# Kernel optimization log

Hardware: AMD Instinct MI355X
Metric: run time of the kernel (lower is better)

Reference implementation:

```python
import jax, jax.numpy as jnp
import numpy as np

D = 256; H = 8; DK = 32; L = 5; FF = 2048; K = 31
EPS_LN = 1e-12  # espnet LayerNorm eps
EPS_BN = 1e-5   # torch BatchNorm1d eps


def _ln(x, g, b):
    mu = x.mean(-1, keepdims=True)
    v = ((x - mu) ** 2).mean(-1, keepdims=True)
    return (x - mu) / jnp.sqrt(v + EPS_LN) * g + b


def _swish(x):
    return x * jax.nn.sigmoid(x)


def _pos_emb(T):
    # espnet RelPositionalEncoding: relative positions T-1 .. -(T-1), length 2T-1
    pos = jnp.arange(T, dtype=jnp.float32)[:, None]
    div = jnp.exp(jnp.arange(0, D, 2, dtype=jnp.float32) * (-np.log(10000.0) / D))[None, :]
    pe_pos = jnp.stack([jnp.sin(pos * div), jnp.cos(pos * div)], -1).reshape(T, D)
    pe_neg = jnp.stack([jnp.sin(-pos * div), jnp.cos(-pos * div)], -1).reshape(T, D)
    return jnp.concatenate([pe_pos[::-1], pe_neg[1:]], 0)  # (2T-1, D)


def _rel_shift(x):
    # x: (B, H, T, 2T-1) -> (B, H, T, T), Transformer-XL style shift
    B, Hh, T, N = x.shape
    x = jnp.pad(x, ((0, 0), (0, 0), (0, 0), (1, 0)))
    x = x.reshape(B, Hh, N + 1, T)[:, :, 1:, :].reshape(B, Hh, T, N)
    return x[..., : (N // 2 + 1)]


def _attn(x, pe, mask, Wq, bq, Wk, bk, Wv, bv, Wo, bo, Wp, pu, pv):
    B, T, _ = x.shape
    q = (x @ Wq.T + bq).reshape(B, T, H, DK)
    k = (x @ Wk.T + bk).reshape(B, T, H, DK).transpose(0, 2, 1, 3)
    v = (x @ Wv.T + bv).reshape(B, T, H, DK).transpose(0, 2, 1, 3)
    p = (pe @ Wp.T).reshape(-1, H, DK)  # (2T-1, H, DK)
    qu = (q + pu).transpose(0, 2, 1, 3)
    qv = (q + pv).transpose(0, 2, 1, 3)
    ac = jnp.einsum('bhtd,bhsd->bhts', qu, k)
    bd = _rel_shift(jnp.einsum('bhtd,nhd->bhtn', qv, p))
    scores = (ac + bd) / np.sqrt(DK)
    m = mask[:, None, :, :]  # (B,1,1,T)
    scores = jnp.where(m, scores, -1e30)
    a = jax.nn.softmax(scores, -1)
    a = jnp.where(m, a, 0.0)
    out = jnp.einsum('bhts,bhsd->bthd', a, v).reshape(B, T, D)
    return out @ Wo.T + bo


def _conv(x, pw1_w, pw1_b, dw_w, dw_b, bn_g, bn_b, pw2_w, pw2_b):
    y = x @ pw1_w.T + pw1_b                      # (B,T,2D)
    a, b = jnp.split(y, 2, -1)
    y = (a * jax.nn.sigmoid(b)).transpose(0, 2, 1)  # GLU -> (B,D,T)
    y = jax.lax.conv_general_dilated(
        y, dw_w[:, None, :], (1,), [(K // 2, K // 2)],
        feature_group_count=D, dimension_numbers=('NCW', 'OIW', 'NCW')
    ) + dw_b[None, :, None]
    mu = y.mean((0, 2), keepdims=True)
    var = ((y - mu) ** 2).mean((0, 2), keepdims=True)  # batch stats (train mode)
    y = (y - mu) / jnp.sqrt(var + EPS_BN) * bn_g[None, :, None] + bn_b[None, :, None]
    y = _swish(y).transpose(0, 2, 1)
    return y @ pw2_w.T + pw2_b


def _forward(xs, Wemb, bemb, ln_in_g, ln_in_b, Wq, bq, Wk, bk, Wv, bv, Wo, bo, Wp,
             pos_u, pos_v, ln1_g, ln1_b, lnc_g, lnc_b, lnf_g, lnf_b, lnfin_g, lnfin_b,
             pw1_w, pw1_b, dw_w, dw_b, bn_g, bn_b, pw2_w, pw2_b,
             ff1_w, ff1_b, ff2_w, ff2_b, after_g, after_b, mask):
    B, T, _ = xs.shape
    x = _ln(xs @ Wemb.T + bemb, ln_in_g, ln_in_b)  # linear input layer + LN
    x = x * np.sqrt(D)                              # rel-pos encoding x-scale
    pe = _pos_emb(T)
    for i in range(L):
        x = x + _attn(_ln(x, ln1_g[i], ln1_b[i]), pe, mask,
                      Wq[i], bq[i], Wk[i], bk[i], Wv[i], bv[i], Wo[i], bo[i],
                      Wp[i], pos_u[i], pos_v[i])
        x = x + _conv(_ln(x, lnc_g[i], lnc_b[i]),
                      pw1_w[i], pw1_b[i], dw_w[i], dw_b[i],
                      bn_g[i], bn_b[i], pw2_w[i], pw2_b[i])
        h = _ln(x, lnf_g[i], lnf_b[i])
        x = x + _swish(h @ ff1_w[i].T + ff1_b[i]) @ ff2_w[i].T + ff2_b[i]
        x = _ln(x, lnfin_g[i], lnfin_b[i])
    x = _ln(x, after_g, after_b)
    return x.sum(1)  # (B, D) sum-pool over time


def setup_inputs() -> dict:
    key = jax.random.key(0)
    ks = iter(jax.random.split(key, 32))
    B, T, IDIM = 8, 1024, 80
    nrm = lambda shp: jax.random.normal(next(ks), shp, jnp.float32) * 0.02
    z = lambda shp: jnp.zeros(shp, jnp.float32)
    o = lambda shp: jnp.ones(shp, jnp.float32)
    return {
        'xs': jax.random.normal(next(ks), (B, T, IDIM), jnp.float32),
        'Wemb': nrm((D, IDIM)), 'bemb': z((D,)),
        'ln_in_g': o((D,)), 'ln_in_b': z((D,)),
        'Wq': nrm((L, D, D)), 'bq': z((L, D)),
        'Wk': nrm((L, D, D)), 'bk': z((L, D)),
        'Wv': nrm((L, D, D)), 'bv': z((L, D)),
        'Wo': nrm((L, D, D)), 'bo': z((L, D)),
        'Wp': nrm((L, D, D)),
        'pos_u': nrm((L, H, DK)), 'pos_v': nrm((L, H, DK)),
        'ln1_g': o((L, D)), 'ln1_b': z((L, D)),
        'lnc_g': o((L, D)), 'lnc_b': z((L, D)),
        'lnf_g': o((L, D)), 'lnf_b': z((L, D)),
        'lnfin_g': o((L, D)), 'lnfin_b': z((L, D)),
        'pw1_w': nrm((L, 2 * D, D)), 'pw1_b': z((L, 2 * D)),
        'dw_w': nrm((L, D, K)), 'dw_b': z((L, D)),
        'bn_g': o((L, D)), 'bn_b': z((L, D)),
        'pw2_w': nrm((L, D, D)), 'pw2_b': z((L, D)),
        'ff1_w': nrm((L, FF, D)), 'ff1_b': z((L, FF)),
        'ff2_w': nrm((L, D, FF)), 'ff2_b': z((L, D)),
        'after_g': o((D,)), 'after_b': z((D,)),
        'mask': jnp.ones((B, 1, T), bool),
    }


def reference(xs, Wemb, bemb, ln_in_g, ln_in_b, Wq, bq, Wk, bk, Wv, bv, Wo, bo, Wp,
              pos_u, pos_v, ln1_g, ln1_b, lnc_g, lnc_b, lnf_g, lnf_b, lnfin_g, lnfin_b,
              pw1_w, pw1_b, dw_w, dw_b, bn_g, bn_b, pw2_w, pw2_b,
              ff1_w, ff1_b, ff2_w, ff2_b, after_g, after_b, mask):
    return _forward(xs, Wemb, bemb, ln_in_g, ln_in_b, Wq, bq, Wk, bk, Wv, bv, Wo, bo, Wp,
                    pos_u, pos_v, ln1_g, ln1_b, lnc_g, lnc_b, lnf_g, lnf_b, lnfin_g, lnfin_b,
                    pw1_w, pw1_b, dw_w, dw_b, bn_g, bn_b, pw2_w, pw2_b,
                    ff1_w, ff1_b, ff2_w, ff2_b, after_g, after_b, mask)
```

## Files before the change

### kernel.cpp

```cpp
#include <hip/hip_runtime.h>
#include <math.h>


#define Bq 8
#define Tq 1024
#define Dq 256
#define Hq 8
#define FFq 2048
#define IDIMq 80
#define ROWS (Bq * Tq)
#define NPOS (2 * Tq - 1)

typedef _Float16 half8 __attribute__((ext_vector_type(8)));
typedef _Float16 half4v __attribute__((ext_vector_type(4)));
typedef _Float16 half2v __attribute__((ext_vector_type(2)));
typedef float floatx4 __attribute__((ext_vector_type(4)));

__device__ __forceinline__ float sigm(float x) { return 1.f / (1.f + __expf(-x)); }

__device__ __forceinline__ float wave_sum64(float v) {
    #pragma unroll
    for (int off = 1; off < 64; off <<= 1) v += __shfl_xor(v, off, 64);
    return v;
}
// ... 51 lines not shown
    const int r0 = blockIdx.x * 8;
    for (int idx = tid; idx < 8 * IDIMq; idx += 256) {
        int r = idx / IDIMq, c = idx % IDIMq;
        xr[r][c] = xs[(size_t)(r0 + r) * IDIMq + c];
    }
    __syncthreads();
    float4 w[20];
    const float4* wp = (const float4*)(Wemb + (size_t)tid * IDIMq);
    #pragma unroll
    for (int i = 0; i < 20; ++i) w[i] = wp[i];
    const float bias = bemb[tid];
    #pragma unroll
    for (int r = 0; r < 8; ++r) {
        float acc = bias;
        const float* x = xr[r];
        #pragma unroll
        for (int i = 0; i < 20; ++i)
            acc += w[i].x * x[4 * i] + w[i].y * x[4 * i + 1]
                 + w[i].z * x[4 * i + 2] + w[i].w * x[4 * i + 3];
        E[(size_t)(r0 + r) * 256 + tid] = acc;
    }
}

__global__ __launch_bounds__(256) void k_lnw(
    const float* __restrict__ Xin, const float* __restrict__ g,
    const float* __restrict__ bb, _Float16* __restrict__ O) {
    const int lane = threadIdx.x & 63;
    const int row = blockIdx.x * 4 + (threadIdx.x >> 6);
    const float4 v = *(const float4*)(Xin + (size_t)row * 256 + lane * 4);
    float mu = wave_sum64(v.x + v.y + v.z + v.w) * (1.f / 256.f);
    float dx = v.x - mu, dy = v.y - mu, dz = v.z - mu, dw = v.w - mu;
    float var = wave_sum64(dx * dx + dy * dy + dz * dz + dw * dw) * (1.f / 256.f);
    float rstd = 1.f / sqrtf(var + 1e-12f);
    const float4 gg = *(const float4*)(g + lane * 4);
    const float4 bv = *(const float4*)(bb + lane * 4);
    half4v o;
    o[0] = (_Float16)(dx * rstd * gg.x + bv.x);
    o[1] = (_Float16)(dy * rstd * gg.y + bv.y);
    o[2] = (_Float16)(dz * rstd * gg.z + bv.z);
    o[3] = (_Float16)(dw * rstd * gg.w + bv.w);
    *(half4v*)(O + (size_t)row * 256 + lane * 4) = o;
}

__global__ __launch_bounds__(256) void k_ln2w(
    const float* __restrict__ Xin, const float* __restrict__ g1,
    const float* __restrict__ b1, float s1,
    const float* __restrict__ g2, const float* __restrict__ b2,
    float* __restrict__ Xout, _Float16* __restrict__ XH) {
    const int lane = threadIdx.x & 63;
    const int row = blockIdx.x * 4 + (threadIdx.x >> 6);
    const float4 v = *(const float4*)(Xin + (size_t)row * 256 + lane * 4);
    float mu = wave_sum64(v.x + v.y + v.z + v.w) * (1.f / 256.f);
    float dx = v.x - mu, dy = v.y - mu, dz = v.z - mu, dw = v.w - mu;
    float var = wave_sum64(dx * dx + dy * dy + dz * dz + dw * dw) * (1.f / 256.f);
    float rstd = 1.f / sqrtf(var + 1e-12f);
    const float4 g1v = *(const float4*)(g1 + lane * 4);
    const float4 b1v = *(const float4*)(b1 + lane * 4);
    float4 y;
    y.x = (dx * rstd * g1v.x + b1v.x) * s1;
    y.y = (dy * rstd * g1v.y + b1v.y) * s1;
    y.z = (dz * rstd * g1v.z + b1v.z) * s1;
    y.w = (dw * rstd * g1v.w + b1v.w) * s1;
    *(float4*)(Xout + (size_t)row * 256 + lane * 4) = y;
    float mu2 = wave_sum64(y.x + y.y + y.z + y.w) * (1.f / 256.f);
    float ex = y.x - mu2, ey = y.y - mu2, ez = y.z - mu2, ew = y.w - mu2;
    float var2 = wave_sum64(ex * ex + ey * ey + ez * ez + ew * ew) * (1.f / 256.f);
    float rstd2 = 1.f / sqrtf(var2 + 1e-12f);
    const float4 g2v = *(const float4*)(g2 + lane * 4);
    const float4 b2v = *(const float4*)(b2 + lane * 4);
    half4v o;
    o[0] = (_Float16)(ex * rstd2 * g2v.x + b2v.x);
    o[1] = (_Float16)(ey * rstd2 * g2v.y + b2v.y);
    o[2] = (_Float16)(ez * rstd2 * g2v.z + b2v.z);
    o[3] = (_Float16)(ew * rstd2 * g2v.w + b2v.w);
    *(half4v*)(XH + (size_t)row * 256 + lane * 4) = o;
}

#define GF_SWISH 1
#define GF_ACC   2
#define GF_F16   4
#define GF_PH    8
#define GF_BNA   16
#define GF_QKV   32
template<int KC>
__global__ __launch_bounds__(256) void k_gemm2(
    const _Float16* __restrict__ A, const _Float16* __restrict__ W,
    const float* __restrict__ bias, const float* __restrict__ bnp,
    float* __restrict__ Cf, _Float16* __restrict__ Ch,
    int M, int N, int ldw, int woff, int flags) {
    const int tid = threadIdx.x;
    const int wave = tid >> 6, lane = tid & 63;
    const int quad = lane >> 4, l16 = lane & 15;
    const int m0 = blockIdx.y * 128 + (wave & 1) * 64;
    const int n0 = blockIdx.x * 64 + (wave >> 1) * 32;
    const _Float16* Ap[4];
    #pragma unroll
    for (int i = 0; i < 4; ++i) {
        int r_ = m0 + 16 * i + l16;
        if (r_ >= M) r_ = M - 1;
        Ap[i] = A + (size_t)r_ * KC + quad * 8;
    }
    const _Float16* Wp0 = W + (size_t)(n0 + l16) * ldw + woff + quad * 8;
    const _Float16* Wp1 = Wp0 + (size_t)16 * ldw;
    floatx4 acc[4][2] = {};
    for (int ko = 0; ko < KC; ko += 256) {
        #pragma unroll
        for (int k1 = 0; k1 < 256 && k1 < KC; k1 += 32) {
            int k0 = ko + k1;
            half8 b0 = *(const half8*)(Wp0 + k0);
            half8 b1 = *(const half8*)(Wp1 + k0);
            float scv[8], shv[8];
            if (flags & GF_BNA) {
                *(float4*)&scv[0] = *(const float4*)(bnp + k0 + quad * 8);
                *(float4*)&scv[4] = *(const float4*)(bnp + k0 + quad * 8 + 4);
                *(float4*)&shv[0] = *(const float4*)(bnp + 256 + k0 + quad * 8);
                *(float4*)&shv[4] = *(const float4*)(bnp + 256 + k0 + quad * 8 + 4);
            }
            #pragma unroll
            for (int i = 0; i < 4; ++i) {
                half8 a = *(const half8*)(Ap[i] + k0);
                if (flags & GF_BNA) {
                    #pragma unroll
                    for (int j = 0; j < 8; ++j) {
                        float f = (float)a[j] * scv[j] + shv[j];
                        a[j] = (_Float16)(f * sigm(f));
                    }
                }
                acc[i][0] = __builtin_amdgcn_mfma_f32_16x16x32_f16(a, b0, acc[i][0], 0, 0, 0);
                acc[i][1] = __builtin_amdgcn_mfma_f32_16x16x32_f16(a, b1, acc[i][1], 0, 0, 0);
            }
        }
    }
    #pragma unroll
    for (int i = 0; i < 4; ++i) {
        #pragma unroll
        for (int j = 0; j < 2; ++j) {
            #pragma unroll
            for (int r = 0; r < 4; ++r) {
                int row = m0 + i * 16 + quad * 4 + r;
                int col = n0 + j * 16 + l16;
                if (row < M) {
                    float v = acc[i][j][r];
                    if (bias) v += bias[col];
                    if (flags & GF_SWISH) v = v * sigm(v);
                    if (flags & GF_PH) {
                        Ch[((size_t)(col >> 5) * 2048 + row) * 32 + (col & 31)] = (_Float16)v;
                    } else if (flags & GF_QKV) {
                        if (col < 256) {
                            Ch[(size_t)row * 256 + col] = (_Float16)v;
                        } else if (col < 512) {
                            int hh = (col - 256) >> 5, d = col & 31;
                            int bb2 = row >> 10, t = row & 1023;
                            Ch[2097152 + (((size_t)(bb2 * 8 + hh) << 10) + t) * 32 + d] = (_Float16)v;
                        } else {
                            Ch[4194304 + (size_t)row * 256 + (col - 512)] = (_Float16)v;
                        }
                    } else {
                        size_t idx = (size_t)row * N + col;
                        if (flags & GF_ACC) Cf[idx] += v;
                        else if (flags & GF_F16) Ch[idx] = (_Float16)v;
                        else Cf[idx] = v;
                    }
                }
            }
        }
    }
}

__global__ __launch_bounds__(256) void k_gemm_glu(
    const _Float16* __restrict__ A, const _Float16* __restrict__ W,
    const float* __restrict__ bias, _Float16* __restrict__ Oh) {
    const int tid = threadIdx.x;
    const int wave = tid >> 6, lane = tid & 63;
    const int quad = lane >> 4, l16 = lane & 15;
    const int m0 = blockIdx.y * 128 + (wave & 1) * 64;
    const int n0 = blockIdx.x * 64 + (wave >> 1) * 32;
    const int K = 256;
    const _Float16* Ap[4];
    #pragma unroll
    for (int i = 0; i < 4; ++i)
        Ap[i] = A + (size_t)(m0 + 16 * i + l16) * K + quad * 8;
    const _Float16* Wa0 = W + (size_t)(n0 + l16) * K + quad * 8;
    const _Float16* Wa1 = Wa0 + (size_t)16 * K;
    const _Float16* Wb0 = Wa0 + (size_t)256 * K;
    const _Float16* Wb1 = Wa1 + (size_t)256 * K;
    floatx4 acc1[4][2] = {}, acc2[4][2] = {};
    #pragma unroll
    for (int k0 = 0; k0 < 256; k0 += 32) {
        half8 b0 = *(const half8*)(Wa0 + k0);
        half8 b1 = *(const half8*)(Wa1 + k0);
        half8 c0 = *(const half8*)(Wb0 + k0);
        half8 c1 = *(const half8*)(Wb1 + k0);
        #pragma unroll
        for (int i = 0; i < 4; ++i) {
            half8 a = *(const half8*)(Ap[i] + k0);
            acc1[i][0] = __builtin_amdgcn_mfma_f32_16x16x32_f16(a, b0, acc1[i][0], 0, 0, 0);
            acc1[i][1] = __builtin_amdgcn_mfma_f32_16x16x32_f16(a, b1, acc1[i][1], 0, 0, 0);
            acc2[i][0] = __builtin_amdgcn_mfma_f32_16x16x32_f16(a, c0, acc2[i][0], 0, 0, 0);
            acc2[i][1] = __builtin_amdgcn_mfma_f32_16x16x32_f16(a, c1, acc2[i][1], 0, 0, 0);
        }
    }
    #pragma unroll
    for (int i = 0; i < 4; ++i) {
        #pragma unroll
        for (int j = 0; j < 2; ++j) {
            #pragma unroll
            for (int r = 0; r < 4; ++r) {
                int row = m0 + i * 16 + quad * 4 + r;
                int col = n0 + j * 16 + l16;
                float a = acc1[i][j][r] + bias[col];
                float g = acc2[i][j][r] + bias[256 + col];
                Oh[(size_t)row * 256 + col] = (_Float16)(a * sigm(g));
            }
        }
    }
}

__global__ __launch_bounds__(256) void k_vtrans(const _Float16* __restrict__ VH,
                                                _Float16* __restrict__ VT) {
    __shared__ _Float16 S[64][264];
    const int r0 = blockIdx.x * 64;
    const int b = r0 >> 10;
    const int tid = threadIdx.x;
    #pragma unroll
    for (int i = 0; i < 8; ++i) {
        int idx = tid + 256 * i;
        int row = idx >> 5, ch = idx & 31;
        uint4 v = *(const uint4*)(VH + (size_t)(r0 + row) * 256 + ch * 8);
        *(uint4*)(&S[row][ch * 8]) = v;
    }
    __syncthreads();
    const int s0 = r0 & 1023;
    _Float16* dst = VT + ((size_t)(b * 8) * 32 + (tid >> 5) * 32 + (tid & 31)) * 1024 + s0;
    #pragma unroll
    for (int p0 = 0; p0 < 64; p0 += 8) {
        half8 t;
        #pragma unroll
        for (int j = 0; j < 8; ++j) {
            int pos = p0 + j;
            int blk = pos >> 5, pl = pos & 31;
            int srow = blk * 32 + (pl >> 1) + 16 * (pl & 1);
            t[j] = S[srow][tid];
        }
        *(half8*)(dst + p0) = t;
    }
}

__global__ __launch_bounds__(256, 4) void k_attn5(
    const _Float16* __restrict__ QH, const _Float16* __restrict__ KH,
    const _Float16* __restrict__ PH, const _Float16* __restrict__ VT,
    const float* __restrict__ pu, const float* __restrict__ pv,
    _Float16* __restrict__ Out) {
    __shared__ __align__(16) _Float16 Pl[4][16 * 40];
    const int tid = threadIdx.x;
    const int wave = tid >> 6, lane = tid & 63;
    const int quad = lane >> 4, l16 = lane & 15;
    const int h = blockIdx.y, b = blockIdx.z;
    const int tb = blockIdx.x * 64 + wave * 16;
    const float scale = 0.17677669529663687f;
    half8 qu_f, qv_f;
    {
        half8 q = *(const half8*)(QH + ((size_t)(b * Tq) + tb + l16) * 256 + h * 32 + quad * 8);
        #pragma unroll
        for (int j = 0; j < 8; ++j) {
            float qf = (float)q[j];
            qu_f[j] = (_Float16)((qf + pu[h * 32 + quad * 8 + j]) * scale);
            qv_f[j] = (_Float16)((qf + pv[h * 32 + quad * 8 + j]) * scale);
        }
    }
    int srcA[4];
    bool selA[4], selB[4];
    #pragma unroll
    for (int r = 0; r < 4; ++r) {
        int tt = quad * 4 + r;
        int cp0 = l16 - tt + 15;
        srcA[r] = quad * 16 + (cp0 & 15);
        selA[r] = (cp0 >> 4) != 0;
        selB[r] = ((cp0 + 16) >> 4) != 1;
    }
    floatx4 o0 = {0.f, 0.f, 0.f, 0.f}, o1 = {0.f, 0.f, 0.f, 0.f};
    float l_r[4] = {0.f, 0.f, 0.f, 0.f};
    const _Float16* Kbase = KH + ((size_t)(b * 8 + h) << 10) * 32 + quad * 8;
    const _Float16* Vbase = VT + ((size_t)(b * 8 + h) * 32 + l16) * 1024 + quad * 8;
    const _Float16* Pbase = PH + (size_t)h * 2048 * 32 + quad * 8;
    const int nb0 = 1023 - tb - 15;
    _Float16* plH = &Pl[wave][0];
    unsigned int* plU = (unsigned int*)plH;
    half8 kb0 = *(const half8*)(Kbase + (size_t)(l16) * 32);
    half8 kb1 = *(const half8*)(Kbase + (size_t)(16 + l16) * 32);
    half8 pb0 = *(const half8*)(Pbase + (size_t)(nb0 + l16) * 32);
    half8 pb1 = *(const half8*)(Pbase + (size_t)(nb0 + 16 + l16) * 32);
    half8 pb2 = *(const half8*)(Pbase + (size_t)(nb0 + 32 + l16) * 32);
    half8 vb0 = *(const half8*)(Vbase);
    half8 vb1 = *(const half8*)(Vbase + 16 * 1024);
    for (int it = 0; it < 32; ++it) {
        const int sbn = (it == 31) ? it * 32 : (it + 1) * 32;
        half8 nk0 = *(const half8*)(Kbase + (size_t)(sbn + l16) * 32);
        half8 nk1 = *(const half8*)(Kbase + (size_t)(sbn + 16 + l16) * 32);
        half8 np0 = *(const half8*)(Pbase + (size_t)(nb0 + sbn + l16) * 32);
        half8 np1 = *(const half8*)(Pbase + (size_t)(nb0 + sbn + 16 + l16) * 32);
        half8 np2 = *(const half8*)(Pbase + (size_t)(nb0 + sbn + 32 + l16) * 32);
        half8 nv0 = *(const half8*)(Vbase + sbn);
        half8 nv1 = *(const half8*)(Vbase + 16 * 1024 + sbn);
        floatx4 z = {0.f, 0.f, 0.f, 0.f};
        floatx4 sc0 = __builtin_amdgcn_mfma_f32_16x16x32_f16(qu_f, kb0, z, 0, 0, 0);
        floatx4 sc1 = __builtin_amdgcn_mfma_f32_16x16x32_f16(qu_f, kb1, z, 0, 0, 0);
        floatx4 d0 = __builtin_amdgcn_mfma_f32_16x16x32_f16(qv_f, pb0, z, 0, 0, 0);
        floatx4 d1 = __builtin_amdgcn_mfma_f32_16x16x32_f16(qv_f, pb1, z, 0, 0, 0);
        floatx4 d2 = __builtin_amdgcn_mfma_f32_16x16x32_f16(qv_f, pb2, z, 0, 0, 0);
        #pragma unroll
        for (int r = 0; r < 4; ++r) {
            half2v pk01; pk01[0] = (_Float16)d0[r]; pk01[1] = (_Float16)d1[r];
            half2v pk12; pk12[0] = (_Float16)d1[r]; pk12[1] = (_Float16)d2[r];
            float gA = __shfl(__builtin_bit_cast(float, pk01), srcA[r]);
            float gB = __shfl(__builtin_bit_cast(float, pk12), srcA[r]);
            half2v hA = __builtin_bit_cast(half2v, gA);
            half2v hB = __builtin_bit_cast(half2v, gB);
            float bd0 = (float)(selA[r] ? hA[1] : hA[0]);
            float bd1 = (float)(selB[r] ? hB[1] : hB[0]);
            float p0 = __expf(sc0[r] + bd0);
            float p1 = __expf(sc1[r] + bd1);
            l_r[r] += p0 + p1;
            half2v pp; pp[0] = (_Float16)p0; pp[1] = (_Float16)p1;
            plU[(quad * 4 + r) * 20 + l16] = __builtin_bit_cast(unsigned int, pp);
        }
        half4v lo = *(const half4v*)(plH + l16 * 40 + quad * 8);
        half4v hi = *(const half4v*)(plH + l16 * 40 + quad * 8 + 4);
        half8 pa;
        pa[0] = lo[0]; pa[1] = lo[1]; pa[2] = lo[2]; pa[3] = lo[3];
        pa[4] = hi[0]; pa[5] = hi[1]; pa[6] = hi[2]; pa[7] = hi[3];
        o0 = __builtin_amdgcn_mfma_f32_16x16x32_f16(pa, vb0, o0, 0, 0, 0);
        o1 = __builtin_amdgcn_mfma_f32_16x16x32_f16(pa, vb1, o1, 0, 0, 0);
        kb0 = nk0; kb1 = nk1; pb0 = np0; pb1 = np1; pb2 = np2; vb0 = nv0; vb1 = nv1;
    }
    #pragma unroll
    for (int r = 0; r < 4; ++r) {
        float l = l_r[r];
        #pragma unroll
        for (int off = 1; off < 16; off <<= 1) l += __shfl_xor(l, off);
        float inv = 1.f / l;
        size_t ob = ((size_t)(b * Tq) + tb + quad * 4 + r) * 256 + h * 32;
        Out[ob + l16] = (_Float16)(o0[r] * inv);
        Out[ob + 16 + l16] = (_Float16)(o1[r] * inv);
    }
}

__global__ __launch_bounds__(256) void k_dwconv4(
    const _Float16* __restrict__ Xin, const float* __restrict__ WT,
    const float* __restrict__ wb, _Float16* __restrict__ Y,
    float* __restrict__ SP, float* __restrict__ SP2) {
    __shared__ float spb[4][256], sp2b[4][256];
    const int tid = threadIdx.x;
    const int cg = tid & 63;
    const int strip = tid >> 6;
    const int row0 = blockIdx.x * 32 + strip * 8;
    const int t0 = row0 & 1023;
    const int c4 = cg * 4;
    const _Float16* xb = Xin + (size_t)(row0 - t0) * 256 + c4;
    float4 bias = *(const float4*)(wb + c4);
    float4 acc[8];
    #pragma unroll
    for (int j = 0; j < 8; ++j) acc[j] = bias;
    float4 win[8];
    #pragma unroll
    for (int j = 0; j < 8; ++j) {
        int t = t0 - 15 + j;
        if (t >= 0 && t < Tq) {
            half4v x = *(const half4v*)(xb + (size_t)t * 256);
            win[j] = make_float4((float)x[0], (float)x[1], (float)x[2], (float)x[3]);
        } else win[j] = make_float4(0.f, 0.f, 0.f, 0.f);
    }
    #pragma unroll
    for (int k = 0; k < 31; ++k) {
        float4 wk = *(const float4*)(WT + (size_t)k * 256 + c4);
        #pragma unroll
        for (int j = 0; j < 8; ++j) {
            acc[j].x += wk.x * win[j].x;
            acc[j].y += wk.y * win[j].y;
            acc[j].z += wk.z * win[j].z;
            acc[j].w += wk.w * win[j].w;
        }
        if (k < 30) {
            int t = t0 - 7 + k;
            float4 nw;
            if (t >= 0 && t < Tq) {
                half4v x = *(const half4v*)(xb + (size_t)t * 256);
                nw = make_float4((float)x[0], (float)x[1], (float)x[2], (float)x[3]);
            } else nw = make_float4(0.f, 0.f, 0.f, 0.f);
            #pragma unroll
            for (int j = 0; j < 7; ++j) win[j] = win[j + 1];
            win[7] = nw;
        }
    }
    float4 s = make_float4(0.f, 0.f, 0.f, 0.f), s2 = make_float4(0.f, 0.f, 0.f, 0.f);
    #pragma unroll
    for (int j = 0; j < 8; ++j) {
        half4v o; o[0] = (_Float16)acc[j].x; o[1] = (_Float16)acc[j].y;
        o[2] = (_Float16)acc[j].z; o[3] = (_Float16)acc[j].w;
        *(half4v*)(Y + (size_t)(row0 + j) * 256 + c4) = o;
        s.x += acc[j].x; s.y += acc[j].y; s.z += acc[j].z; s.w += acc[j].w;
        s2.x += acc[j].x * acc[j].x; s2.y += acc[j].y * acc[j].y;
        s2.z += acc[j].z * acc[j].z; s2.w += acc[j].w * acc[j].w;
    }
    *(float4*)&spb[strip][c4] = s;
    *(float4*)&sp2b[strip][c4] = s2;
    __syncthreads();
    if (tid < 256) {
        SP[blockIdx.x * 256 + tid] = spb[0][tid] + spb[1][tid] + spb[2][tid] + spb[3][tid];
        SP2[blockIdx.x * 256 + tid] = sp2b[0][tid] + sp2b[1][tid] + sp2b[2][tid] + sp2b[3][tid];
    }
}

__global__ void k_bns2(const float* __restrict__ SP, const float* __restrict__ SP2,
                       const float* __restrict__ g, const float* __restrict__ bb,
                       float* __restrict__ BNS) {
    int c = blockIdx.x;
    int p = threadIdx.x;
    __shared__ float rs[256], rs2[256];
    rs[p] = SP[p * 256 + c];
    rs2[p] = SP2[p * 256 + c];
    __syncthreads();
    for (int st = 128; st > 0; st >>= 1) {
        if (p < st) { rs[p] += rs[p + st]; rs2[p] += rs2[p + st]; }
        __syncthreads();
    }
    if (p == 0) {
        float mu = rs[0] / (float)ROWS;
// ... 2 lines not shown
        float sc = rstd * g[c];
        BNS[c] = sc;
        BNS[256 + c] = bb[c] - mu * sc;
    }
}

__global__ void k_partial(const _Float16* __restrict__ Xl, float* __restrict__ Pt) {
    int chunk = blockIdx.x, b = blockIdx.y, d = threadIdx.x;
    float s = 0.f;
    int t0 = chunk * 32;
    for (int t = 0; t < 32; ++t)
        s += (float)Xl[((size_t)b * Tq + t0 + t) * Dq + d];
    Pt[((size_t)b * 32 + chunk) * Dq + d] = s;
}
__global__ void k_finalsum(const float* __restrict__ Pt, float* __restrict__ out) {
    int b = blockIdx.x, d = threadIdx.x;
    float s = 0.f;
    for (int c = 0; c < 32; ++c)
        s += Pt[((size_t)b * 32 + c) * Dq + d];
    out[(size_t)b * Dq + d] = s;
}

extern "C" void kernel_launch(void* const* d_in, const int* in_sizes, int n_in,
                              void* d_out, int out_size, void* d_ws, size_t ws_size,
                              hipStream_t stream) {
    const float* xs      = (const float*)d_in[0];
    const float* Wemb    = (const float*)d_in[1];
    const float* bemb    = (const float*)d_in[2];
    const float* ln_in_g = (const float*)d_in[3];
    const float* ln_in_b = (const float*)d_in[4];
    const float* Wq      = (const float*)d_in[5];
    const float* bq      = (const float*)d_in[6];
    const float* Wk      = (const float*)d_in[7];
    const float* bk      = (const float*)d_in[8];
    const float* Wv      = (const float*)d_in[9];
    const float* bv      = (const float*)d_in[10];
    const float* Wo      = (const float*)d_in[11];
    const float* bo      = (const float*)d_in[12];
    const float* Wp      = (const float*)d_in[13];
    const float* pos_u   = (const float*)d_in[14];
    const float* pos_v   = (const float*)d_in[15];
    const float* ln1_g   = (const float*)d_in[16];
    const float* ln1_b   = (const float*)d_in[17];
    const float* lnc_g   = (const float*)d_in[18];
    const float* lnc_b   = (const float*)d_in[19];
    const float* lnf_g   = (const float*)d_in[20];
    const float* lnf_b   = (const float*)d_in[21];
    const float* lnfin_g = (const float*)d_in[22];
    const float* lnfin_b = (const float*)d_in[23];
    const float* pw1_w   = (const float*)d_in[24];
    const float* pw1_b   = (const float*)d_in[25];
    const float* dw_w    = (const float*)d_in[26];
    const float* dw_b    = (const float*)d_in[27];
    const float* bn_g    = (const float*)d_in[28];
    const float* bn_b    = (const float*)d_in[29];
    const float* pw2_w   = (const float*)d_in[30];
    const float* pw2_b   = (const float*)d_in[31];
    const float* ff1_w   = (const float*)d_in[32];
    const float* ff1_b   = (const float*)d_in[33];
    const float* ff2_w   = (const float*)d_in[34];
    const float* ff2_b   = (const float*)d_in[35];
    const float* after_g = (const float*)d_in[36];
    const float* after_b = (const float*)d_in[37];

    char* wsb = (char*)d_ws;
    const size_t MB = (size_t)1 << 20;
    float*     X    = (float*)(wsb + 0);
    _Float16*  XH   = (_Float16*)(wsb + 8 * MB);
    _Float16*  PEh  = (_Float16*)(wsb + 12 * MB);
    float*     BNS  = (float*)(wsb + 13 * MB);
    float*     SP   = (float*)(wsb + 13 * MB + 4096);
    float*     SP2  = (float*)(wsb + 13 * MB + 4096 + 262144);
    float*     BQKV = (float*)(wsb + 13 * MB + 4096 + 524288);
    float*     PART = (float*)(wsb + 13 * MB + 4096 + 524288 + 16384);
    float*     WT   = (float*)(wsb + 13 * MB + 4096 + 524288 + 16384 + 262144);
    _Float16*  WH   = (_Float16*)(wsb + 14 * MB);
    _Float16*  QKVd = (_Float16*)(wsb + 30 * MB);
    _Float16*  T1h  = (_Float16*)(wsb + 42 * MB);
    _Float16*  T2h  = (_Float16*)(wsb + 46 * MB);
    float*     E    = (float*)(wsb + 42 * MB);
    _Float16*  FFHh = (_Float16*)(wsb + 30 * MB);
    _Float16*  PHp  = (_Float16*)(wsb + 50 * MB);
    _Float16*  VT   = (_Float16*)(wsb + 51 * MB);

    _Float16*  QH   = QKVd;
    _Float16*  KH   = QKVd + 2097152;
    _Float16*  VH   = QKVd + 4194304;

    _Float16* WoH   = WH;
    _Float16* WpH   = WH + 327680;
    _Float16* pw1H  = WH + 655360;
    _Float16* pw2H  = WH + 1310720;
    _Float16* ff1H  = WH + 1638400;
    _Float16* ff2H  = WH + 4259840;
    _Float16* WqkvH = WH + 6881280;

    auto f2h = [&](const float* in, _Float16* out, size_t n) {
        int n4 = (int)(n >> 2);
        k_f2h<<<dim3((n4 + 255) / 256), dim3(256), 0, stream>>>(in, out, n4);
    };

    f2h(Wo, WoH, 5 * 65536);
    f2h(Wp, WpH, 5 * 65536);
    f2h(pw1_w, pw1H, 5 * 131072);
    f2h(pw2_w, pw2H, 5 * 65536);
    f2h(ff1_w, ff1H, (size_t)5 * 524288);
    f2h(ff2_w, ff2H, (size_t)5 * 524288);
    k_pack_qkv<<<dim3(960), dim3(256), 0, stream>>>(Wq, Wk, Wv, bq, bk, bv, WqkvH, BQKV);
    k_wtrans<<<dim3(5), dim3(256), 0, stream>>>(dw_w, WT);
    k_pe<<<dim3(NPOS), dim3(256), 0, stream>>>(PEh);
    k_embed_mm<<<dim3(ROWS / 8), dim3(256), 0, stream>>>(xs, Wemb, bemb, E);
    k_ln2w<<<dim3(ROWS / 4), dim3(256), 0, stream>>>(
        E, ln_in_g, ln_in_b, 16.f, ln1_g, ln1_b, X, XH);

    for (int l = 0; l < 5; ++l) {
        k_gemm2<256><<<dim3(12, 64), dim3(256), 0, stream>>>(
            XH, WqkvH + (size_t)l * 196608, BQKV + l * 768, nullptr, nullptr, QKVd,
            ROWS, 768, 256, 0, GF_QKV);
        k_gemm2<256><<<dim3(4, 16), dim3(256), 0, stream>>>(
            PEh, WpH + (size_t)l * 65536, nullptr, nullptr, nullptr, PHp,
            NPOS, 256, 256, 0, GF_F16 | GF_PH);
        k_vtrans<<<dim3(ROWS / 64), dim3(256), 0, stream>>>(VH, VT);
        k_attn5<<<dim3(Tq / 64, Hq, Bq), dim3(256), 0, stream>>>(
            QH, KH, PHp, VT, pos_u + l * Dq, pos_v + l * Dq, T1h);
        k_gemm2<256><<<dim3(4, 64), dim3(256), 0, stream>>>(
            T1h, WoH + (size_t)l * 65536, bo + l * Dq, nullptr, X, nullptr,
            ROWS, 256, 256, 0, GF_ACC);
        k_lnw<<<dim3(ROWS / 4), dim3(256), 0, stream>>>(X, lnc_g + l * Dq, lnc_b + l * Dq, XH);
        k_gemm_glu<<<dim3(4, ROWS / 128), dim3(256), 0, stream>>>(
            XH, pw1H + (size_t)l * 131072, pw1_b + l * 512, T1h);
        k_dwconv4<<<dim3(ROWS / 32), dim3(256), 0, stream>>>(
            T1h, WT + (size_t)l * 31 * 256, dw_b + l * Dq, T2h, SP, SP2);
        k_bns2<<<dim3(256), dim3(256), 0, stream>>>(SP, SP2, bn_g + l * Dq, bn_b + l * Dq, BNS);
        k_gemm2<256><<<dim3(4, 64), dim3(256), 0, stream>>>(
            T2h, pw2H + (size_t)l * 65536, pw2_b + l * Dq, BNS, X, nullptr,
            ROWS, 256, 256, 0, GF_ACC | GF_BNA);
        k_lnw<<<dim3(ROWS / 4), dim3(256), 0, stream>>>(X, lnf_g + l * Dq, lnf_b + l * Dq, XH);
        const _Float16* f1 = ff1H + (size_t)l * 524288;
        const _Float16* f2 = ff2H + (size_t)l * 524288;
        k_gemm2<256><<<dim3(16, 64), dim3(256), 0, stream>>>(
            XH, f1, ff1_b + l * FFq, nullptr, nullptr, FFHh,
            ROWS, 1024, 256, 0, GF_SWISH | GF_F16);
        k_gemm2<1024><<<dim3(4, 64), dim3(256), 0, stream>>>(
            FFHh, f2, ff2_b + l * Dq, nullptr, X, nullptr,
            ROWS, 256, 2048, 0, GF_ACC);
        k_gemm2<256><<<dim3(16, 64), dim3(256), 0, stream>>>(
            XH, f1 + (size_t)1024 * 256, ff1_b + l * FFq + 1024, nullptr, nullptr, FFHh,
            ROWS, 1024, 256, 0, GF_SWISH | GF_F16);
        k_gemm2<1024><<<dim3(4, 64), dim3(256), 0, stream>>>(
            FFHh, f2, nullptr, nullptr, X, nullptr,
            ROWS, 256, 2048, 1024, GF_ACC);
        const float* g2 = (l < 4) ? (ln1_g + (l + 1) * Dq) : after_g;
        const float* b2 = (l < 4) ? (ln1_b + (l + 1) * Dq) : after_b;
        k_ln2w<<<dim3(ROWS / 4), dim3(256), 0, stream>>>(
            X, lnfin_g + l * Dq, lnfin_b + l * Dq, 1.f, g2, b2, X, XH);
    }

    k_partial<<<dim3(32, Bq), dim3(256), 0, stream>>>(XH, PART);
    k_finalsum<<<dim3(Bq), dim3(256), 0, stream>>>(PART, (float*)d_out);
}
```

Before: 2.001 ms.

## Split attention keys across two blocks and shrink GEMM M-tile for N=256

```diff
diff --git a/kernel.cpp b/kernel.cpp
--- a/kernel.cpp
+++ b/kernel.cpp
@@ -157,27 +157,28 @@
 #define GF_PH    8
 #define GF_BNA   16
 #define GF_QKV   32
-template<int KC>
+template<int KC, int TM>
 __global__ __launch_bounds__(256) void k_gemm2(
     const _Float16* __restrict__ A, const _Float16* __restrict__ W,
     const float* __restrict__ bias, const float* __restrict__ bnp,
     float* __restrict__ Cf, _Float16* __restrict__ Ch,
     int M, int N, int ldw, int woff, int flags) {
+    constexpr int NF = TM / 32;
     const int tid = threadIdx.x;
     const int wave = tid >> 6, lane = tid & 63;
     const int quad = lane >> 4, l16 = lane & 15;
-    const int m0 = blockIdx.y * 128 + (wave & 1) * 64;
+    const int m0 = blockIdx.y * TM + (wave & 1) * (TM / 2);
     const int n0 = blockIdx.x * 64 + (wave >> 1) * 32;
-    const _Float16* Ap[4];
-    #pragma unroll
-    for (int i = 0; i < 4; ++i) {
+    const _Float16* Ap[NF];
+    #pragma unroll
+    for (int i = 0; i < NF; ++i) {
         int r_ = m0 + 16 * i + l16;
         if (r_ >= M) r_ = M - 1;
         Ap[i] = A + (size_t)r_ * KC + quad * 8;
     }
     const _Float16* Wp0 = W + (size_t)(n0 + l16) * ldw + woff + quad * 8;
     const _Float16* Wp1 = Wp0 + (size_t)16 * ldw;
-    floatx4 acc[4][2] = {};
+    floatx4 acc[NF][2] = {};
     for (int ko = 0; ko < KC; ko += 256) {
         #pragma unroll
         for (int k1 = 0; k1 < 256 && k1 < KC; k1 += 32) {
@@ -192,7 +193,7 @@
                 *(float4*)&shv[4] = *(const float4*)(bnp + 256 + k0 + quad * 8 + 4);
             }
             #pragma unroll
-            for (int i = 0; i < 4; ++i) {
+            for (int i = 0; i < NF; ++i) {
                 half8 a = *(const half8*)(Ap[i] + k0);
                 if (flags & GF_BNA) {
                     #pragma unroll
@@ -207,7 +208,7 @@
         }
     }
     #pragma unroll
-    for (int i = 0; i < 4; ++i) {
+    for (int i = 0; i < NF; ++i) {
         #pragma unroll
         for (int j = 0; j < 2; ++j) {
             #pragma unroll
@@ -321,17 +322,19 @@
     }
 }
 
-__global__ __launch_bounds__(256, 4) void k_attn5(
+__global__ __launch_bounds__(256, 4) void k_attn6(
     const _Float16* __restrict__ QH, const _Float16* __restrict__ KH,
     const _Float16* __restrict__ PH, const _Float16* __restrict__ VT,
     const float* __restrict__ pu, const float* __restrict__ pv,
-    _Float16* __restrict__ Out) {
+    _Float16* __restrict__ OP, float* __restrict__ LP) {
     __shared__ __align__(16) _Float16 Pl[4][16 * 40];
     const int tid = threadIdx.x;
     const int wave = tid >> 6, lane = tid & 63;
     const int quad = lane >> 4, l16 = lane & 15;
+    const int tblk = blockIdx.x & 15, shalf = blockIdx.x >> 4;
     const int h = blockIdx.y, b = blockIdx.z;
-    const int tb = blockIdx.x * 64 + wave * 16;
+    const int tb = tblk * 64 + wave * 16;
+    const int s0 = shalf * 512;
     const float scale = 0.17677669529663687f;
     half8 qu_f, qv_f;
     {
@@ -361,15 +364,16 @@
     const int nb0 = 1023 - tb - 15;
     _Float16* plH = &Pl[wave][0];
     unsigned int* plU = (unsigned int*)plH;
-    half8 kb0 = *(const half8*)(Kbase + (size_t)(l16) * 32);
-    half8 kb1 = *(const half8*)(Kbase + (size_t)(16 + l16) * 32);
-    half8 pb0 = *(const half8*)(Pbase + (size_t)(nb0 + l16) * 32);
-    half8 pb1 = *(const half8*)(Pbase + (size_t)(nb0 + 16 + l16) * 32);
-    half8 pb2 = *(const half8*)(Pbase + (size_t)(nb0 + 32 + l16) * 32);
-    half8 vb0 = *(const half8*)(Vbase);
-    half8 vb1 = *(const half8*)(Vbase + 16 * 1024);
-    for (int it = 0; it < 32; ++it) {
-        const int sbn = (it == 31) ? it * 32 : (it + 1) * 32;
+    half8 kb0 = *(const half8*)(Kbase + (size_t)(s0 + l16) * 32);
+    half8 kb1 = *(const half8*)(Kbase + (size_t)(s0 + 16 + l16) * 32);
+    half8 pb0 = *(const half8*)(Pbase + (size_t)(nb0 + s0 + l16) * 32);
+    half8 pb1 = *(const half8*)(Pbase + (size_t)(nb0 + s0 + 16 + l16) * 32);
+    half8 pb2 = *(const half8*)(Pbase + (size_t)(nb0 + s0 + 32 + l16) * 32);
+    half8 vb0 = *(const half8*)(Vbase + s0);
+    half8 vb1 = *(const half8*)(Vbase + 16 * 1024 + s0);
+    for (int it = 0; it < 16; ++it) {
+        const int sb = s0 + it * 32;
+        const int sbn = (it == 15) ? sb : sb + 32;
         half8 nk0 = *(const half8*)(Kbase + (size_t)(sbn + l16) * 32);
         half8 nk1 = *(const half8*)(Kbase + (size_t)(sbn + 16 + l16) * 32);
         half8 np0 = *(const half8*)(Pbase + (size_t)(nb0 + sbn + l16) * 32);
@@ -408,16 +412,39 @@
         o1 = __builtin_amdgcn_mfma_f32_16x16x32_f16(pa, vb1, o1, 0, 0, 0);
         kb0 = nk0; kb1 = nk1; pb0 = np0; pb1 = np1; pb2 = np2; vb0 = nv0; vb1 = nv1;
     }
+    _Float16* Ob = OP + (size_t)shalf * 2097152;
+    float* Lb = LP + (size_t)shalf * 65536;
     #pragma unroll
     for (int r = 0; r < 4; ++r) {
         float l = l_r[r];
         #pragma unroll
         for (int off = 1; off < 16; off <<= 1) l += __shfl_xor(l, off);
         float inv = 1.f / l;
-        size_t ob = ((size_t)(b * Tq) + tb + quad * 4 + r) * 256 + h * 32;
-        Out[ob + l16] = (_Float16)(o0[r] * inv);
-        Out[ob + 16 + l16] = (_Float16)(o1[r] * inv);
-    }
+        int row = b * Tq + tb + quad * 4 + r;
+        size_t ob = (size_t)row * 256 + h * 32;
+        Ob[ob + l16] = (_Float16)(o0[r] * inv);
+        Ob[ob + 16 + l16] = (_Float16)(o1[r] * inv);
+        if (l16 == 0) Lb[row * 8 + h] = l;
+    }
+}
+
+__global__ __launch_bounds__(256) void k_acomb(
+    const _Float16* __restrict__ OP, const float* __restrict__ LP,
+    _Float16* __restrict__ Out) {
+    const int lane = threadIdx.x & 63;
+    const int row = blockIdx.x * 4 + (threadIdx.x >> 6);
+    const int h = lane >> 3;
+    float l0 = LP[row * 8 + h];
+    float l1 = LP[65536 + row * 8 + h];
+    float inv = 1.f / (l0 + l1);
+    float w0 = l0 * inv, w1 = l1 * inv;
+    half4v a = *(const half4v*)(OP + (size_t)row * 256 + lane * 4);
+    half4v b = *(const half4v*)(OP + 2097152 + (size_t)row * 256 + lane * 4);
+    half4v o;
+    #pragma unroll
+    for (int j = 0; j < 4; ++j)
+        o[j] = (_Float16)(w0 * (float)a[j] + w1 * (float)b[j]);
+    *(half4v*)(Out + (size_t)row * 256 + lane * 4) = o;
 }
 
 __global__ __launch_bounds__(256) void k_dwconv4(
@@ -586,6 +613,8 @@
     _Float16*  FFHh = (_Float16*)(wsb + 30 * MB);
     _Float16*  PHp  = (_Float16*)(wsb + 50 * MB);
     _Float16*  VT   = (_Float16*)(wsb + 51 * MB);
+    _Float16*  OP   = (_Float16*)(wsb + 55 * MB);
+    float*     LP   = (float*)(wsb + 63 * MB);
 
     _Float16*  QH   = QKVd;
     _Float16*  KH   = QKVd + 2097152;
@@ -618,16 +647,17 @@
         E, ln_in_g, ln_in_b, 16.f, ln1_g, ln1_b, X, XH);
 
     for (int l = 0; l < 5; ++l) {
-        k_gemm2<256><<<dim3(12, 64), dim3(256), 0, stream>>>(
+        k_gemm2<256, 128><<<dim3(12, 64), dim3(256), 0, stream>>>(
             XH, WqkvH + (size_t)l * 196608, BQKV + l * 768, nullptr, nullptr, QKVd,
             ROWS, 768, 256, 0, GF_QKV);
-        k_gemm2<256><<<dim3(4, 16), dim3(256), 0, stream>>>(
+        k_gemm2<256, 128><<<dim3(4, 16), dim3(256), 0, stream>>>(
             PEh, WpH + (size_t)l * 65536, nullptr, nullptr, nullptr, PHp,
             NPOS, 256, 256, 0, GF_F16 | GF_PH);
         k_vtrans<<<dim3(ROWS / 64), dim3(256), 0, stream>>>(VH, VT);
-        k_attn5<<<dim3(Tq / 64, Hq, Bq), dim3(256), 0, stream>>>(
-            QH, KH, PHp, VT, pos_u + l * Dq, pos_v + l * Dq, T1h);
-        k_gemm2<256><<<dim3(4, 64), dim3(256), 0, stream>>>(
+        k_attn6<<<dim3(32, Hq, Bq), dim3(256), 0, stream>>>(
+            QH, KH, PHp, VT, pos_u + l * Dq, pos_v + l * Dq, OP, LP);
+        k_acomb<<<dim3(ROWS / 4), dim3(256), 0, stream>>>(OP, LP, T1h);
+        k_gemm2<256, 64><<<dim3(4, 128), dim3(256), 0, stream>>>(
             T1h, WoH + (size_t)l * 65536, bo + l * Dq, nullptr, X, nullptr,
             ROWS, 256, 256, 0, GF_ACC);
         k_lnw<<<dim3(ROWS / 4), dim3(256), 0, stream>>>(X, lnc_g + l * Dq, lnc_b + l * Dq, XH);
@@ -636,22 +666,22 @@
         k_dwconv4<<<dim3(ROWS / 32), dim3(256), 0, stream>>>(
             T1h, WT + (size_t)l * 31 * 256, dw_b + l * Dq, T2h, SP, SP2);
         k_bns2<<<dim3(256), dim3(256), 0, stream>>>(SP, SP2, bn_g + l * Dq, bn_b + l * Dq, BNS);
-        k_gemm2<256><<<dim3(4, 64), dim3(256), 0, stream>>>(
+        k_gemm2<256, 64><<<dim3(4, 128), dim3(256), 0, stream>>>(
             T2h, pw2H + (size_t)l * 65536, pw2_b + l * Dq, BNS, X, nullptr,
             ROWS, 256, 256, 0, GF_ACC | GF_BNA);
         k_lnw<<<dim3(ROWS / 4), dim3(256), 0, stream>>>(X, lnf_g + l * Dq, lnf_b + l * Dq, XH);
         const _Float16* f1 = ff1H + (size_t)l * 524288;
         const _Float16* f2 = ff2H + (size_t)l * 524288;
-        k_gemm2<256><<<dim3(16, 64), dim3(256), 0, stream>>>(
+        k_gemm2<256, 128><<<dim3(16, 64), dim3(256), 0, stream>>>(
             XH, f1, ff1_b + l * FFq, nullptr, nullptr, FFHh,
             ROWS, 1024, 256, 0, GF_SWISH | GF_F16);
-        k_gemm2<1024><<<dim3(4, 64), dim3(256), 0, stream>>>(
+        k_gemm2<1024, 64><<<dim3(4, 128), dim3(256), 0, stream>>>(
             FFHh, f2, ff2_b + l * Dq, nullptr, X, nullptr,
             ROWS, 256, 2048, 0, GF_ACC);
-        k_gemm2<256><<<dim3(16, 64), dim3(256), 0, stream>>>(
+        k_gemm2<256, 128><<<dim3(16, 64), dim3(256), 0, stream>>>(
             XH, f1 + (size_t)1024 * 256, ff1_b + l * FFq + 1024, nullptr, nullptr, FFHh,
             ROWS, 1024, 256, 0, GF_SWISH | GF_F16);
-        k_gemm2<1024><<<dim3(4, 64), dim3(256), 0, stream>>>(
+        k_gemm2<1024, 64><<<dim3(4, 128), dim3(256), 0, stream>>>(
             FFHh, f2, nullptr, nullptr, X, nullptr,
             ROWS, 256, 2048, 1024, GF_ACC);
         const float* g2 = (l < 4) ? (ln1_g + (l + 1) * Dq) : after_g;
```

New measurement: 1.919 ms. 4.1% less time.

## Add 128x128 GEMM tile for wide-N outputs, shrink M tile, software-pipeline attention MFMAs

Applied to the files above, without the earlier changes.

```diff
diff --git a/kernel.cpp b/kernel.cpp
--- a/kernel.cpp
+++ b/kernel.cpp
@@ -157,27 +157,28 @@
 #define GF_PH    8
 #define GF_BNA   16
 #define GF_QKV   32
-template<int KC>
+template<int KC, int TM>
 __global__ __launch_bounds__(256) void k_gemm2(
     const _Float16* __restrict__ A, const _Float16* __restrict__ W,
     const float* __restrict__ bias, const float* __restrict__ bnp,
     float* __restrict__ Cf, _Float16* __restrict__ Ch,
     int M, int N, int ldw, int woff, int flags) {
+    constexpr int NF = TM / 32;
     const int tid = threadIdx.x;
     const int wave = tid >> 6, lane = tid & 63;
     const int quad = lane >> 4, l16 = lane & 15;
-    const int m0 = blockIdx.y * 128 + (wave & 1) * 64;
+    const int m0 = blockIdx.y * TM + (wave & 1) * (TM / 2);
     const int n0 = blockIdx.x * 64 + (wave >> 1) * 32;
-    const _Float16* Ap[4];
-    #pragma unroll
-    for (int i = 0; i < 4; ++i) {
+    const _Float16* Ap[NF];
+    #pragma unroll
+    for (int i = 0; i < NF; ++i) {
         int r_ = m0 + 16 * i + l16;
         if (r_ >= M) r_ = M - 1;
         Ap[i] = A + (size_t)r_ * KC + quad * 8;
     }
     const _Float16* Wp0 = W + (size_t)(n0 + l16) * ldw + woff + quad * 8;
     const _Float16* Wp1 = Wp0 + (size_t)16 * ldw;
-    floatx4 acc[4][2] = {};
+    floatx4 acc[NF][2] = {};
     for (int ko = 0; ko < KC; ko += 256) {
         #pragma unroll
         for (int k1 = 0; k1 < 256 && k1 < KC; k1 += 32) {
@@ -192,7 +193,7 @@
                 *(float4*)&shv[4] = *(const float4*)(bnp + 256 + k0 + quad * 8 + 4);
             }
             #pragma unroll
-            for (int i = 0; i < 4; ++i) {
+            for (int i = 0; i < NF; ++i) {
                 half8 a = *(const half8*)(Ap[i] + k0);
                 if (flags & GF_BNA) {
                     #pragma unroll
@@ -207,7 +208,7 @@
         }
     }
     #pragma unroll
-    for (int i = 0; i < 4; ++i) {
+    for (int i = 0; i < NF; ++i) {
         #pragma unroll
         for (int j = 0; j < 2; ++j) {
             #pragma unroll
@@ -220,22 +221,75 @@
                     if (flags & GF_SWISH) v = v * sigm(v);
                     if (flags & GF_PH) {
                         Ch[((size_t)(col >> 5) * 2048 + row) * 32 + (col & 31)] = (_Float16)v;
-                    } else if (flags & GF_QKV) {
-                        if (col < 256) {
-                            Ch[(size_t)row * 256 + col] = (_Float16)v;
-                        } else if (col < 512) {
-                            int hh = (col - 256) >> 5, d = col & 31;
-                            int bb2 = row >> 10, t = row & 1023;
-                            Ch[2097152 + (((size_t)(bb2 * 8 + hh) << 10) + t) * 32 + d] = (_Float16)v;
-                        } else {
-                            Ch[4194304 + (size_t)row * 256 + (col - 512)] = (_Float16)v;
-                        }
                     } else {
                         size_t idx = (size_t)row * N + col;
                         if (flags & GF_ACC) Cf[idx] += v;
                         else if (flags & GF_F16) Ch[idx] = (_Float16)v;
                         else Cf[idx] = v;
                     }
+                }
+            }
+        }
+    }
+}
+
+template<int KC>
+__global__ __launch_bounds__(256, 2) void k_gemm3(
+    const _Float16* __restrict__ A, const _Float16* __restrict__ W,
+    const float* __restrict__ bias, _Float16* __restrict__ Ch,
+    int M, int N, int flags) {
+    const int tid = threadIdx.x;
+    const int wave = tid >> 6, lane = tid & 63;
+    const int quad = lane >> 4, l16 = lane & 15;
+    const int m0 = blockIdx.y * 128 + (wave & 1) * 64;
+    const int n0 = blockIdx.x * 128 + (wave >> 1) * 64;
+    const _Float16* Ap[4];
+    const _Float16* Wp[4];
+    #pragma unroll
+    for (int i = 0; i < 4; ++i)
+        Ap[i] = A + (size_t)(m0 + 16 * i + l16) * KC + quad * 8;
+    #pragma unroll
+    for (int j = 0; j < 4; ++j)
+        Wp[j] = W + (size_t)(n0 + 16 * j + l16) * KC + quad * 8;
+    floatx4 acc[4][4] = {};
+    #pragma unroll
+    for (int k0 = 0; k0 < KC; k0 += 32) {
+        half8 b0 = *(const half8*)(Wp[0] + k0);
+        half8 b1 = *(const half8*)(Wp[1] + k0);
+        half8 b2 = *(const half8*)(Wp[2] + k0);
+        half8 b3 = *(const half8*)(Wp[3] + k0);
+        #pragma unroll
+        for (int i = 0; i < 4; ++i) {
+            half8 a = *(const half8*)(Ap[i] + k0);
+            acc[i][0] = __builtin_amdgcn_mfma_f32_16x16x32_f16(a, b0, acc[i][0], 0, 0, 0);
+            acc[i][1] = __builtin_amdgcn_mfma_f32_16x16x32_f16(a, b1, acc[i][1], 0, 0, 0);
+            acc[i][2] = __builtin_amdgcn_mfma_f32_16x16x32_f16(a, b2, acc[i][2], 0, 0, 0);
+            acc[i][3] = __builtin_amdgcn_mfma_f32_16x16x32_f16(a, b3, acc[i][3], 0, 0, 0);
+        }
+    }
+    #pragma unroll
+    for (int i = 0; i < 4; ++i) {
+        #pragma unroll
+        for (int j = 0; j < 4; ++j) {
+            #pragma unroll
+            for (int r = 0; r < 4; ++r) {
+                int row = m0 + i * 16 + quad * 4 + r;
+                int col = n0 + j * 16 + l16;
+                float v = acc[i][j][r];
+                if (bias) v += bias[col];
+                if (flags & GF_SWISH) v = v * sigm(v);
+                if (flags & GF_QKV) {
+                    if (col < 256) {
+                        Ch[(size_t)row * 256 + col] = (_Float16)v;
+                    } else if (col < 512) {
+                        int hh = (col - 256) >> 5, d = col & 31;
+                        int bb2 = row >> 10, t = row & 1023;
+                        Ch[2097152 + (((size_t)(bb2 * 8 + hh) << 10) + t) * 32 + d] = (_Float16)v;
+                    } else {
+                        Ch[4194304 + (size_t)row * 256 + (col - 512)] = (_Float16)v;
+                    }
+                } else {
+                    Ch[(size_t)row * N + col] = (_Float16)v;
                 }
             }
         }
@@ -321,7 +375,7 @@
     }
 }
 
-__global__ __launch_bounds__(256, 4) void k_attn5(
+__global__ __launch_bounds__(256, 4) void k_attn7(
     const _Float16* __restrict__ QH, const _Float16* __restrict__ KH,
     const _Float16* __restrict__ PH, const _Float16* __restrict__ VT,
     const float* __restrict__ pu, const float* __restrict__ pv,
@@ -361,13 +415,23 @@
     const int nb0 = 1023 - tb - 15;
     _Float16* plH = &Pl[wave][0];
     unsigned int* plU = (unsigned int*)plH;
-    half8 kb0 = *(const half8*)(Kbase + (size_t)(l16) * 32);
-    half8 kb1 = *(const half8*)(Kbase + (size_t)(16 + l16) * 32);
-    half8 pb0 = *(const half8*)(Pbase + (size_t)(nb0 + l16) * 32);
-    half8 pb1 = *(const half8*)(Pbase + (size_t)(nb0 + 16 + l16) * 32);
-    half8 pb2 = *(const half8*)(Pbase + (size_t)(nb0 + 32 + l16) * 32);
-    half8 vb0 = *(const half8*)(Vbase);
-    half8 vb1 = *(const half8*)(Vbase + 16 * 1024);
+    half8 vb0, vb1;
+    floatx4 sc0, sc1, d0, d1, d2;
+    {
+        half8 kb0 = *(const half8*)(Kbase + (size_t)l16 * 32);
+        half8 kb1 = *(const half8*)(Kbase + (size_t)(16 + l16) * 32);
+        half8 pb0 = *(const half8*)(Pbase + (size_t)(nb0 + l16) * 32);
+        half8 pb1 = *(const half8*)(Pbase + (size_t)(nb0 + 16 + l16) * 32);
+        half8 pb2 = *(const half8*)(Pbase + (size_t)(nb0 + 32 + l16) * 32);
+        vb0 = *(const half8*)(Vbase);
+        vb1 = *(const half8*)(Vbase + 16 * 1024);
+        floatx4 z = {0.f, 0.f, 0.f, 0.f};
+        sc0 = __builtin_amdgcn_mfma_f32_16x16x32_f16(qu_f, kb0, z, 0, 0, 0);
+        sc1 = __builtin_amdgcn_mfma_f32_16x16x32_f16(qu_f, kb1, z, 0, 0, 0);
+        d0 = __builtin_amdgcn_mfma_f32_16x16x32_f16(qv_f, pb0, z, 0, 0, 0);
+        d1 = __builtin_amdgcn_mfma_f32_16x16x32_f16(qv_f, pb1, z, 0, 0, 0);
+        d2 = __builtin_amdgcn_mfma_f32_16x16x32_f16(qv_f, pb2, z, 0, 0, 0);
+    }
     for (int it = 0; it < 32; ++it) {
         const int sbn = (it == 31) ? it * 32 : (it + 1) * 32;
         half8 nk0 = *(const half8*)(Kbase + (size_t)(sbn + l16) * 32);
@@ -377,12 +441,6 @@
         half8 np2 = *(const half8*)(Pbase + (size_t)(nb0 + sbn + 32 + l16) * 32);
         half8 nv0 = *(const half8*)(Vbase + sbn);
         half8 nv1 = *(const half8*)(Vbase + 16 * 1024 + sbn);
-        floatx4 z = {0.f, 0.f, 0.f, 0.f};
-        floatx4 sc0 = __builtin_amdgcn_mfma_f32_16x16x32_f16(qu_f, kb0, z, 0, 0, 0);
-        floatx4 sc1 = __builtin_amdgcn_mfma_f32_16x16x32_f16(qu_f, kb1, z, 0, 0, 0);
-        floatx4 d0 = __builtin_amdgcn_mfma_f32_16x16x32_f16(qv_f, pb0, z, 0, 0, 0);
-        floatx4 d1 = __builtin_amdgcn_mfma_f32_16x16x32_f16(qv_f, pb1, z, 0, 0, 0);
-        floatx4 d2 = __builtin_amdgcn_mfma_f32_16x16x32_f16(qv_f, pb2, z, 0, 0, 0);
         #pragma unroll
         for (int r = 0; r < 4; ++r) {
             half2v pk01; pk01[0] = (_Float16)d0[r]; pk01[1] = (_Float16)d1[r];
@@ -399,6 +457,12 @@
             half2v pp; pp[0] = (_Float16)p0; pp[1] = (_Float16)p1;
             plU[(quad * 4 + r) * 20 + l16] = __builtin_bit_cast(unsigned int, pp);
         }
+        floatx4 z = {0.f, 0.f, 0.f, 0.f};
+        floatx4 t0 = __builtin_amdgcn_mfma_f32_16x16x32_f16(qu_f, nk0, z, 0, 0, 0);
+        floatx4 t1 = __builtin_amdgcn_mfma_f32_16x16x32_f16(qu_f, nk1, z, 0, 0, 0);
+        floatx4 t2 = __builtin_amdgcn_mfma_f32_16x16x32_f16(qv_f, np0, z, 0, 0, 0);
+        floatx4 t3 = __builtin_amdgcn_mfma_f32_16x16x32_f16(qv_f, np1, z, 0, 0, 0);
+        floatx4 t4 = __builtin_amdgcn_mfma_f32_16x16x32_f16(qv_f, np2, z, 0, 0, 0);
         half4v lo = *(const half4v*)(plH + l16 * 40 + quad * 8);
         half4v hi = *(const half4v*)(plH + l16 * 40 + quad * 8 + 4);
         half8 pa;
@@ -406,7 +470,8 @@
         pa[4] = hi[0]; pa[5] = hi[1]; pa[6] = hi[2]; pa[7] = hi[3];
         o0 = __builtin_amdgcn_mfma_f32_16x16x32_f16(pa, vb0, o0, 0, 0, 0);
         o1 = __builtin_amdgcn_mfma_f32_16x16x32_f16(pa, vb1, o1, 0, 0, 0);
-        kb0 = nk0; kb1 = nk1; pb0 = np0; pb1 = np1; pb2 = np2; vb0 = nv0; vb1 = nv1;
+        sc0 = t0; sc1 = t1; d0 = t2; d1 = t3; d2 = t4;
+        vb0 = nv0; vb1 = nv1;
     }
     #pragma unroll
     for (int r = 0; r < 4; ++r) {
@@ -618,16 +683,15 @@
         E, ln_in_g, ln_in_b, 16.f, ln1_g, ln1_b, X, XH);
 
     for (int l = 0; l < 5; ++l) {
-        k_gemm2<256><<<dim3(12, 64), dim3(256), 0, stream>>>(
-            XH, WqkvH + (size_t)l * 196608, BQKV + l * 768, nullptr, nullptr, QKVd,
-            ROWS, 768, 256, 0, GF_QKV);
-        k_gemm2<256><<<dim3(4, 16), dim3(256), 0, stream>>>(
+        k_gemm3<256><<<dim3(6, 64), dim3(256), 0, stream>>>(
+            XH, WqkvH + (size_t)l * 196608, BQKV + l * 768, QKVd, ROWS, 768, GF_QKV);
+        k_gemm2<256, 128><<<dim3(4, 16), dim3(256), 0, stream>>>(
             PEh, WpH + (size_t)l * 65536, nullptr, nullptr, nullptr, PHp,
             NPOS, 256, 256, 0, GF_F16 | GF_PH);
         k_vtrans<<<dim3(ROWS / 64), dim3(256), 0, stream>>>(VH, VT);
-        k_attn5<<<dim3(Tq / 64, Hq, Bq), dim3(256), 0, stream>>>(
+        k_attn7<<<dim3(Tq / 64, Hq, Bq), dim3(256), 0, stream>>>(
             QH, KH, PHp, VT, pos_u + l * Dq, pos_v + l * Dq, T1h);
-        k_gemm2<256><<<dim3(4, 64), dim3(256), 0, stream>>>(
+        k_gemm2<256, 64><<<dim3(4, 128), dim3(256), 0, stream>>>(
             T1h, WoH + (size_t)l * 65536, bo + l * Dq, nullptr, X, nullptr,
             ROWS, 256, 256, 0, GF_ACC);
         k_lnw<<<dim3(ROWS / 4), dim3(256), 0, stream>>>(X, lnc_g + l * Dq, lnc_b + l * Dq, XH);
@@ -636,22 +700,21 @@
         k_dwconv4<<<dim3(ROWS / 32), dim3(256), 0, stream>>>(
             T1h, WT + (size_t)l * 31 * 256, dw_b + l * Dq, T2h, SP, SP2);
         k_bns2<<<dim3(256), dim3(256), 0, stream>>>(SP, SP2, bn_g + l * Dq, bn_b + l * Dq, BNS);
-        k_gemm2<256><<<dim3(4, 64), dim3(256), 0, stream>>>(
+        k_gemm2<256, 64><<<dim3(4, 128), dim3(256), 0, stream>>>(
             T2h, pw2H + (size_t)l * 65536, pw2_b + l * Dq, BNS, X, nullptr,
             ROWS, 256, 256, 0, GF_ACC | GF_BNA);
         k_lnw<<<dim3(ROWS / 4), dim3(256), 0, stream>>>(X, lnf_g + l * Dq, lnf_b + l * Dq, XH);
         const _Float16* f1 = ff1H + (size_t)l * 524288;
         const _Float16* f2 = ff2H + (size_t)l * 524288;
-        k_gemm2<256><<<dim3(16, 64), dim3(256), 0, stream>>>(
-            XH, f1, ff1_b + l * FFq, nullptr, nullptr, FFHh,
-            ROWS, 1024, 256, 0, GF_SWISH | GF_F16);
-        k_gemm2<1024><<<dim3(4, 64), dim3(256), 0, stream>>>(
+        k_gemm3<256><<<dim3(8, 64), dim3(256), 0, stream>>>(
+            XH, f1, ff1_b + l * FFq, FFHh, ROWS, 1024, GF_SWISH | GF_F16);
+        k_gemm2<1024, 64><<<dim3(4, 128), dim3(256), 0, stream>>>(
             FFHh, f2, ff2_b + l * Dq, nullptr, X, nullptr,
             ROWS, 256, 2048, 0, GF_ACC);
-        k_gemm2<256><<<dim3(16, 64), dim3(256), 0, stream>>>(
-            XH, f1 + (size_t)1024 * 256, ff1_b + l * FFq + 1024, nullptr, nullptr, FFHh,
-            ROWS, 1024, 256, 0, GF_SWISH | GF_F16);
-        k_gemm2<1024><<<dim3(4, 64), dim3(256), 0, stream>>>(
+        k_gemm3<256><<<dim3(8, 64), dim3(256), 0, stream>>>(
+            XH, f1 + (size_t)1024 * 256, ff1_b + l * FFq + 1024, FFHh, ROWS, 1024,
+            GF_SWISH | GF_F16);
+        k_gemm2<1024, 64><<<dim3(4, 128), dim3(256), 0, stream>>>(
             FFHh, f2, nullptr, nullptr, X, nullptr,
             ROWS, 256, 2048, 1024, GF_ACC);
         const float* g2 = (l < 4) ? (ln1_g + (l + 1) * Dq) : after_g;
```

After: 1.908 ms. 4.6% less time.
